# Kernel tuning notes

Hardware: AMD Instinct MI355X
Metric: run time of the kernel (lower is better)

The kernel has to match this reference:

```python
import jax, jax.numpy as jnp
import numpy as np
import math

N_, LQ, C = 8, 300, 256
HEADS, NLVL, NPTS = 8, 4, 8
D_HEAD = C // HEADS
LEVELS = [(128, 128), (64, 64), (32, 32), (16, 16)]
LEN_IN = sum(h * w for h, w in LEVELS)
STARTS = np.cumsum([0] + [h * w for h, w in LEVELS])
MH, MW = 128, 128  # reference mask resolution


def _offset_bias():
    # replicates _reset_parameters grid init for sampling_offsets.bias
    thetas = np.arange(HEADS, dtype=np.float32) * (2.0 * math.pi / HEADS)
    grid = np.stack([np.cos(thetas), np.sin(thetas)], -1)  # (H, 2)
    grid = grid / np.abs(grid).max(-1, keepdims=True)
    grid = np.tile(grid[:, None, None, :], (1, NLVL, NPTS, 1))  # (H, L, P, 2)
    for i in range(NPTS):
        grid[:, :, i, :] *= i + 1
    return jnp.asarray(grid.reshape(-1), dtype=jnp.float32)


def setup_inputs() -> dict:
    key = jax.random.key(0)
    ks = jax.random.split(key, 8)
    query = jax.random.normal(ks[0], (N_, LQ, C), dtype=jnp.float32)
    reference_bboxs = jax.random.normal(ks[1], (N_, LQ, 4), dtype=jnp.float32)
    reference_masks = jax.random.normal(ks[2], (N_, LQ, MH, MW), dtype=jnp.float32)
    input_flatten = jax.random.normal(ks[3], (N_, LEN_IN, C), dtype=jnp.float32)
    input_spatial_shapes = jnp.asarray(LEVELS, dtype=jnp.int64)
    input_level_start_index = jnp.asarray(STARTS[:-1], dtype=jnp.int64)
    input_padding_mask = jnp.zeros((N_, LEN_IN), dtype=bool)
    s = 1.0 / math.sqrt(C)
    W_off = jax.random.normal(ks[4], (C, HEADS * NLVL * NPTS * 2), dtype=jnp.float32) * 0.01
    b_off = _offset_bias()
    W_attn = jax.random.normal(ks[5], (C, HEADS * NLVL * NPTS), dtype=jnp.float32) * 0.01
    b_attn = jnp.zeros((HEADS * NLVL * NPTS,), dtype=jnp.float32)
    W_val = jax.random.normal(ks[6], (C, C), dtype=jnp.float32) * s
    b_val = jnp.zeros((C,), dtype=jnp.float32)
    W_out = jax.random.normal(ks[7], (C, C), dtype=jnp.float32) * s
    b_out = jnp.zeros((C,), dtype=jnp.float32)
    return dict(query=query, reference_bboxs=reference_bboxs, reference_masks=reference_masks,
                mask_threshold=0, input_flatten=input_flatten,
                input_spatial_shapes=input_spatial_shapes,
                input_level_start_index=input_level_start_index,
                input_padding_mask=input_padding_mask,
                W_off=W_off, b_off=b_off, W_attn=W_attn, b_attn=b_attn,
                W_val=W_val, b_val=b_val, W_out=W_out, b_out=b_out)


def get_bounding_boxes(masks):
    # masks: (N, Q, H, W) bool -> normalized (cx, cy, w, h), (N, Q, 4)
    H, W = masks.shape[-2:]
    xs = masks.any(-2)  # (N, Q, W)
    ys = masks.any(-1)  # (N, Q, H)
    xi = jnp.arange(W, dtype=jnp.float32)
    yi = jnp.arange(H, dtype=jnp.float32)
    x_min = jnp.min(jnp.where(xs, xi, float(W)), -1)
    x_max = jnp.max(jnp.where(xs, xi, -1.0), -1)
    y_min = jnp.min(jnp.where(ys, yi, float(H)), -1)
    y_max = jnp.max(jnp.where(ys, yi, -1.0), -1)
    nonempty = xs.any(-1)
    x0, x1 = x_min / W, (x_max + 1.0) / W
    y0, y1 = y_min / H, (y_max + 1.0) / H
    box = jnp.stack([(x0 + x1) * 0.5, (y0 + y1) * 0.5, x1 - x0, y1 - y0], -1)
    return jnp.where(nonempty[..., None], box, 0.0)


def check_points_in_mask(mask, points):
    # mask: (N, Q, H, W) bool; points: (N, Q, P, 2) normalized -> (N, Q, P) float
    N, Q, H, W = mask.shape
    px = jnp.clip((points[..., 0] * W).astype(jnp.int32), 0, W - 1)
    py = jnp.clip((points[..., 1] * H).astype(jnp.int32), 0, H - 1)
    idx = py * W + px  # (N, Q, P)
    flat = mask.reshape(N, Q, H * W)
    return jnp.take_along_axis(flat, idx, axis=2).astype(jnp.float32)


def ms_deform_attn_core(value, sampling_locations, attention_weights):
    # value: (N, Len_in, heads, d); loc: (N, Lq, heads, L, P, 2); w: (N, Lq, heads, L, P)
    N, Lq = sampling_locations.shape[:2]
    out = jnp.zeros((N, Lq, HEADS, D_HEAD), dtype=value.dtype)
    for l, (Hl, Wl) in enumerate(LEVELS):
        v = value[:, STARTS[l]:STARTS[l + 1]].transpose(0, 2, 1, 3)  # (N, heads, Hl*Wl, d)
        loc = sampling_locations[:, :, :, l]  # (N, Lq, heads, P, 2)
        # grid_sample(align_corners=False): pixel = loc*size - 0.5
        px = loc[..., 0] * Wl - 0.5
        py = loc[..., 1] * Hl - 0.5
        x0 = jnp.floor(px); y0 = jnp.floor(py)
        wx1 = px - x0; wy1 = py - y0
        x0i = x0.astype(jnp.int32); y0i = y0.astype(jnp.int32)

        def gather(xi, yi):
            valid = (xi >= 0) & (xi < Wl) & (yi >= 0) & (yi < Hl)
            idx = jnp.clip(yi, 0, Hl - 1) * Wl + jnp.clip(xi, 0, Wl - 1)  # (N, Lq, heads, P)
            idx2 = idx.transpose(0, 2, 1, 3).reshape(N, HEADS, Lq * NPTS)
            g = jnp.take_along_axis(v, idx2[..., None], axis=2)  # (N, heads, Lq*P, d)
            g = g.reshape(N, HEADS, Lq, NPTS, D_HEAD).transpose(0, 2, 1, 3, 4)
            return g * valid[..., None].astype(g.dtype)

        samp = (gather(x0i, y0i) * ((1 - wx1) * (1 - wy1))[..., None]
                + gather(x0i + 1, y0i) * (wx1 * (1 - wy1))[..., None]
                + gather(x0i, y0i + 1) * ((1 - wx1) * wy1)[..., None]
                + gather(x0i + 1, y0i + 1) * (wx1 * wy1)[..., None])
        out = out + jnp.einsum('nqhpd,nqhp->nqhd', samp, attention_weights[:, :, :, l])
    return out.reshape(N, Lq, C)


def reference(query, reference_bboxs, reference_masks, mask_threshold, input_flatten,
              input_spatial_shapes, input_level_start_index, input_padding_mask,
              W_off, b_off, W_attn, b_attn, W_val, b_val, W_out, b_out):
    N, Lq, _ = query.shape
    value = input_flatten @ W_val + b_val
    value = jnp.where(input_padding_mask[..., None], 0.0, value)
    value = value.reshape(N, LEN_IN, HEADS, D_HEAD)
    offsets = (query @ W_off + b_off).reshape(N, Lq, HEADS, NLVL, NPTS, 2)
    attw = (query @ W_attn + b_attn).reshape(N, Lq, HEADS, NLVL, NPTS)
    ref_masks = reference_masks > 0
    box = get_bounding_boxes(ref_masks)  # (N, Lq, 4) normalized cxcywh
    ctr = box[:, :, None, None, None, :2]
    wh = box[:, :, None, None, None, 2:]
    loc = ctr + offsets / NPTS * wh * 0.5  # (N, Lq, heads, L, P, 2)
    pin = check_points_in_mask(ref_masks, loc.reshape(N, Lq, -1, 2))
    attw = attw * pin.reshape(N, Lq, HEADS, NLVL, NPTS)
    attw = jax.nn.softmax(attw.reshape(N, Lq, HEADS, NLVL * NPTS), -1)
    attw = attw.reshape(N, Lq, HEADS, NLVL, NPTS)
    out = ms_deform_attn_core(value, loc, attw)
    return out @ W_out + b_out
```

## Files before the change

kernel.cpp:

```cpp
#include <hip/hip_runtime.h>
#include <math.h>

#define NB    8
#define LQ    300
#define CC    256
#define HEADS 8
#define NLVL  4
#define NPTS  8
#define DH    32
#define LEN_IN 21760
#define NQ    (NB*LQ)
#define MH    128
#define MW    128

typedef __attribute__((ext_vector_type(8))) short bf16x8;
typedef __attribute__((ext_vector_type(8))) unsigned short ushort8;
typedef __attribute__((ext_vector_type(4))) float f32x4;
typedef unsigned short ushort;
typedef unsigned int uint;

#define AS1 __attribute__((address_space(1)))
#define AS3 __attribute__((address_space(3)))

static __device__ __forceinline__ ushort f2bf(float f) {
    uint u = __builtin_bit_cast(uint, f);
    uint r = (u + 0x7fffu + ((u >> 16) & 1u)) >> 16;
    return (ushort)r;
}

__global__ void transpose_cast_w(const float* __restrict__ W, ushort* __restrict__ Bt) {
    int n = blockIdx.x, k = threadIdx.x;
    Bt[n * CC + k] = f2bf(W[(size_t)k * CC + n]);
}

__global__ __launch_bounds__(256) void gemm_mfma_value(
    const float* __restrict__ A, const ushort* __restrict__ Bt,
    const float* __restrict__ bias, float* __restrict__ C, int M)
{
    __shared__ ushort As[128 * 32];
    __shared__ ushort Bs[128 * 32];
    const int tid  = threadIdx.x;
    const int wave = tid >> 6, lane = tid & 63;
    const int bm = blockIdx.x * 128;
    const int bn = blockIdx.y * 128;
    const int wm = (wave >> 1) * 64, wn = (wave & 1) * 64;

    f32x4 acc[4][4] = {};

    const int am = tid >> 1, ak = (tid & 1) * 16;
    const float* aptr = A + (size_t)(bm + am) * CC + ak;
    ushort* as_dst = &As[am * 32 + ak];

    AS3 char* bs_base = (AS3 char*)Bs;

    const int fr = lane & 15, kg = lane >> 4;

    for (int kt = 0; kt < 8; ++kt) {
        const float* ap = aptr + kt * 32;
        float4 f0 = *(const float4*)(ap + 0);
        float4 f1 = *(const float4*)(ap + 4);
        float4 f2 = *(const float4*)(ap + 8);
        float4 f3 = *(const float4*)(ap + 12);
        ushort8 u0, u1;
        u0[0]=f2bf(f0.x); u0[1]=f2bf(f0.y); u0[2]=f2bf(f0.z); u0[3]=f2bf(f0.w);
        u0[4]=f2bf(f1.x); u0[5]=f2bf(f1.y); u0[6]=f2bf(f1.z); u0[7]=f2bf(f1.w);
        u1[0]=f2bf(f2.x); u1[1]=f2bf(f2.y); u1[2]=f2bf(f2.z); u1[3]=f2bf(f2.w);
        u1[4]=f2bf(f3.x); u1[5]=f2bf(f3.y); u1[6]=f2bf(f3.z); u1[7]=f2bf(f3.w);
        *(ushort8*)(as_dst + 0) = u0;
        *(ushort8*)(as_dst + 8) = u1;
        #pragma unroll
        for (int j = 0; j < 2; ++j) {
            int c = wave * 128 + j * 64 + lane;
            const ushort* g = Bt + (size_t)(bn + (c >> 2)) * CC + kt * 32 + (c & 3) * 8;
            __builtin_amdgcn_global_load_lds((const AS1 void*)g,
                                             (AS3 void*)(bs_base + (wave * 128 + j * 64) * 16),
                                             16, 0, 0);
        }
        __syncthreads();
        bf16x8 af[4], bfv[4];
        #pragma unroll
        for (int i = 0; i < 4; ++i)
            af[i] = *(const bf16x8*)&As[(wm + i * 16 + fr) * 32 + kg * 8];
        #pragma unroll
        for (int j = 0; j < 4; ++j)
            bfv[j] = *(const bf16x8*)&Bs[(wn + j * 16 + fr) * 32 + kg * 8];
        #pragma unroll
        for (int i = 0; i < 4; ++i)
            #pragma unroll
            for (int j = 0; j < 4; ++j)
                acc[i][j] = __builtin_amdgcn_mfma_f32_16x16x32_bf16(af[i], bfv[j], acc[i][j], 0, 0, 0);
        __syncthreads();
    }

    const int col0 = lane & 15, rq = (lane >> 4) * 4;
    #pragma unroll
    for (int j = 0; j < 4; ++j) {
        const int col = bn + wn + j * 16 + col0;
        const float bv = bias[col];
        #pragma unroll
        for (int i = 0; i < 4; ++i) {
            const int row = bm + wm + i * 16 + rq;
            #pragma unroll
            for (int r = 0; r < 4; ++r)
                C[(size_t)(row + r) * CC + col] = acc[i][j][r] + bv;
        }
    }
}

#define TM 64
#define TN 64
#define TK 16

__global__ __launch_bounds__(256) void gemm_bias_kernel(
    const float* __restrict__ A, const float* __restrict__ B,
    const float* __restrict__ bias, float* __restrict__ Cmat,
    int M, int N, int K)
{
    __shared__ float As[TK][TM + 4];
    __shared__ float Bs[TK][TN + 4];
    const int tid = threadIdx.x;
    const int bm = blockIdx.x * TM;
    const int bn = blockIdx.y * TN;
    const int tm = (tid >> 4) << 2;
    const int tn = (tid & 15) << 2;
    float acc[4][4] = {};

    for (int k0 = 0; k0 < K; k0 += TK) {
        #pragma unroll
        for (int i = 0; i < 4; ++i) {
            int idx = tid + i * 256;
            int m = idx >> 4;
            int k = idx & 15;
            int gm = bm + m;
            float v = 0.f;
            if (gm < M) v = A[(size_t)gm * K + k0 + k];
            As[k][m] = v;
        }
        #pragma unroll
        for (int i = 0; i < 4; ++i) {
            int idx = tid + i * 256;
            int k = idx >> 6;
            int n = idx & 63;
            int gn = bn + n;
            float v = 0.f;
            if (gn < N) v = B[(size_t)(k0 + k) * N + gn];
            Bs[k][n] = v;
        }
        __syncthreads();
        #pragma unroll
        for (int k = 0; k < TK; ++k) {
            float a[4], b[4];
            #pragma unroll
            for (int i = 0; i < 4; ++i) a[i] = As[k][tm + i];
            #pragma unroll
            for (int j = 0; j < 4; ++j) b[j] = Bs[k][tn + j];
            #pragma unroll
            for (int i = 0; i < 4; ++i)
                #pragma unroll
                for (int j = 0; j < 4; ++j)
                    acc[i][j] = fmaf(a[i], b[j], acc[i][j]);
        }
        __syncthreads();
    }

    #pragma unroll
    for (int i = 0; i < 4; ++i) {
        int m = bm + tm + i;
        if (m >= M) continue;
        #pragma unroll
        for (int j = 0; j < 4; ++j) {
            int n = bn + tn + j;
            if (n < N) Cmat[(size_t)m * N + n] = acc[i][j] + bias[n];
        }
    }
}

__global__ __launch_bounds__(256) void fused_sample_kernel(
    const float* __restrict__ masks,
    const float* __restrict__ value,
    const float* __restrict__ offs,
    const float* __restrict__ attw,
    float* __restrict__ samp)
{
    const int b   = blockIdx.x;
    const int n   = b / LQ;
    const int tid = threadIdx.x;
    const float* mask = masks + (size_t)b * (MH * MW);

    int wmin = MW, wmax = -1, hmin = MH, hmax = -1;
    const float4* m4 = (const float4*)mask;
    for (int i = tid; i < (MH * MW) / 4; i += 256) {
        float4 v = m4[i];
        int base = i << 2;
        int h = base >> 7;
        int w0 = base & 127;
        bool a0 = v.x > 0.f, a1 = v.y > 0.f, a2 = v.z > 0.f, a3 = v.w > 0.f;
        if (a0 | a1 | a2 | a3) { hmin = min(hmin, h); hmax = max(hmax, h); }
        if (a0) { wmin = min(wmin, w0);     wmax = max(wmax, w0);     }
        if (a1) { wmin = min(wmin, w0 + 1); wmax = max(wmax, w0 + 1); }
        if (a2) { wmin = min(wmin, w0 + 2); wmax = max(wmax, w0 + 2); }
        if (a3) { wmin = min(wmin, w0 + 3); wmax = max(wmax, w0 + 3); }
    }
    #pragma unroll
    for (int off = 32; off; off >>= 1) {
        wmin = min(wmin, __shfl_xor(wmin, off));
        wmax = max(wmax, __shfl_xor(wmax, off));
        hmin = min(hmin, __shfl_xor(hmin, off));
        hmax = max(hmax, __shfl_xor(hmax, off));
    }
    __shared__ int s_wmin[4], s_wmax[4], s_hmin[4], s_hmax[4];
    __shared__ float s_box[4];
    const int wave = tid >> 6;
    if ((tid & 63) == 0) {
        s_wmin[wave] = wmin; s_wmax[wave] = wmax;
        s_hmin[wave] = hmin; s_hmax[wave] = hmax;
    }
    __syncthreads();
    if (tid == 0) {
        int a = MW, bx = -1, c = MH, d = -1;
        for (int i = 0; i < 4; ++i) {
            a = min(a, s_wmin[i]); bx = max(bx, s_wmax[i]);
            c = min(c, s_hmin[i]); d = max(d, s_hmax[i]);
        }
        if (bx >= 0) {
            float x0 = a * (1.f / MW), x1 = (bx + 1) * (1.f / MW);
            float y0 = c * (1.f / MH), y1 = (d + 1) * (1.f / MH);
            s_box[0] = (x0 + x1) * 0.5f;
            s_box[1] = (y0 + y1) * 0.5f;
            s_box[2] = x1 - x0;
            s_box[3] = y1 - y0;
        } else {
            s_box[0] = s_box[1] = s_box[2] = s_box[3] = 0.f;
        }
    }
    __syncthreads();
    const float cx = s_box[0], cy = s_box[1], whx = s_box[2], why = s_box[3];

    const float ox = offs[(size_t)b * 512 + tid * 2 + 0];
    const float oy = offs[(size_t)b * 512 + tid * 2 + 1];
    const float lx = cx + ox * (1.f / NPTS) * whx * 0.5f;
    const float ly = cy + oy * (1.f / NPTS) * why * 0.5f;
    int px = (int)(lx * MW); px = min(max(px, 0), MW - 1);
    int py = (int)(ly * MH); py = min(max(py, 0), MH - 1);
    const float pin = (mask[py * MW + px] > 0.f) ? 1.f : 0.f;
    const float logit = attw[(size_t)b * 256 + tid] * pin;
    float mx = logit;
    #pragma unroll
    for (int off = 16; off; off >>= 1) mx = fmaxf(mx, __shfl_xor(mx, off, 32));
    const float e = expf(logit - mx);
    float ssum = e;
    #pragma unroll
    for (int off = 16; off; off >>= 1) ssum += __shfl_xor(ssum, off, 32);
    const float w = e / ssum;

    __shared__ float s_lx[256], s_ly[256], s_w[256];
    s_lx[tid] = lx; s_ly[tid] = ly; s_w[tid] = w;
    __syncthreads();

    const int h = tid >> 5, d = tid & 31;
    const int dims[4]   = {128, 64, 32, 16};
    const int starts[4] = {0, 16384, 20480, 21504};
    const float* vbase = value + (size_t)n * LEN_IN * CC + h * DH + d;
    float acc = 0.f;
    #pragma unroll
    for (int l = 0; l < NLVL; ++l) {
        const int Hl = dims[l], Wl = dims[l], st = starts[l];
        #pragma unroll
        for (int p = 0; p < NPTS; ++p) {
            const int pt = (h * NLVL + l) * NPTS + p;
            const float plx = s_lx[pt], ply = s_ly[pt], pw = s_w[pt];
            const float fx = plx * Wl - 0.5f;
            const float fy = ply * Hl - 0.5f;
            const float x0f = floorf(fx), y0f = floorf(fy);
            const float wx = fx - x0f, wy = fy - y0f;
            const int x0 = (int)x0f, y0 = (int)y0f;
            const int x1 = x0 + 1, y1 = y0 + 1;
            const bool xv0 = (x0 >= 0) && (x0 < Wl);
            const bool xv1 = (x1 >= 0) && (x1 < Wl);
            const bool yv0 = (y0 >= 0) && (y0 < Hl);
            const bool yv1 = (y1 >= 0) && (y1 < Hl);
            float v00 = 0.f, v01 = 0.f, v10 = 0.f, v11 = 0.f;
            if (yv0) {
                const float* row = vbase + (size_t)(st + y0 * Wl) * CC;
                if (xv0) v00 = row[(size_t)x0 * CC];
                if (xv1) v01 = row[(size_t)x1 * CC];
            }
            if (yv1) {
                const float* row = vbase + (size_t)(st + y1 * Wl) * CC;
                if (xv0) v10 = row[(size_t)x0 * CC];
                if (xv1) v11 = row[(size_t)x1 * CC];
            }
            const float bil = v00 * (1.f - wx) * (1.f - wy)
                            + v01 * wx * (1.f - wy)
                            + v10 * (1.f - wx) * wy
                            + v11 * wx * wy;
            acc = fmaf(pw, bil, acc);
        }
    }
    samp[(size_t)b * 256 + tid] = acc;
}

extern "C" void kernel_launch(void* const* d_in, const int* in_sizes, int n_in,
                              void* d_out, int out_size, void* d_ws, size_t ws_size,
                              hipStream_t stream)
{
    const float* query  = (const float*)d_in[0];
    const float* masks  = (const float*)d_in[2];
    const float* flat   = (const float*)d_in[4];
    const float* W_off  = (const float*)d_in[8];
    const float* b_off  = (const float*)d_in[9];
    const float* W_attn = (const float*)d_in[10];
    const float* b_attn = (const float*)d_in[11];
    const float* W_val  = (const float*)d_in[12];
    const float* b_val  = (const float*)d_in[13];
    const float* W_out  = (const float*)d_in[14];
    const float* b_out  = (const float*)d_in[15];
    float* out = (float*)d_out;

    float*  ws    = (float*)d_ws;
    float*  value = ws;
    float*  offs  = value + (size_t)NB * LEN_IN * CC;
    float*  attw  = offs + (size_t)NQ * 512;
    float*  samp  = attw + (size_t)NQ * 256;
    ushort* Bt    = (ushort*)(samp + (size_t)NQ * 256);

    const int Mval = NB * LEN_IN;

    transpose_cast_w<<<CC, CC, 0, stream>>>(W_val, Bt);
    gemm_mfma_value<<<dim3(Mval / 128, CC / 128), 256, 0, stream>>>(
        flat, Bt, b_val, value, Mval);
    gemm_bias_kernel<<<dim3((NQ + TM - 1) / TM, 512 / TN), 256, 0, stream>>>(
        query, W_off, b_off, offs, NQ, 512, CC);
    gemm_bias_kernel<<<dim3((NQ + TM - 1) / TM, CC / TN), 256, 0, stream>>>(
        query, W_attn, b_attn, attw, NQ, CC, CC);
    fused_sample_kernel<<<NQ, 256, 0, stream>>>(masks, value, offs, attw, samp);
    gemm_bias_kernel<<<dim3((NQ + TM - 1) / TM, CC / TN), 256, 0, stream>>>(
        samp, W_out, b_out, out, NQ, CC, CC);
}
```

Measured before the change: 679.7 us.

## Store value projection in bf16 and split bbox from sampling with level-parallel threads

The value GEMM now writes its output as bf16 instead of fp32, which halves the writeback of the large value tensor and the gather traffic in the sampler. The fused kernel is split in two. A bbox kernel fully unrolls the mask scan, and a 512-thread sample kernel splits the four levels across two thread halves and combines them through shared memory. Bilinear loads become branchless, using clamped indices and validity weights. Rounding value to bf16 adds precision error in the sampled output.

```diff
diff --git a/kernel.cpp b/kernel.cpp
--- a/kernel.cpp
+++ b/kernel.cpp
@@ -27,6 +27,9 @@
     uint r = (u + 0x7fffu + ((u >> 16) & 1u)) >> 16;
     return (ushort)r;
 }
+static __device__ __forceinline__ float bf2f(ushort u) {
+    return __builtin_bit_cast(float, ((uint)u) << 16);
+}
 
 __global__ void transpose_cast_w(const float* __restrict__ W, ushort* __restrict__ Bt) {
     int n = blockIdx.x, k = threadIdx.x;
@@ -35,7 +38,7 @@
 
 __global__ __launch_bounds__(256) void gemm_mfma_value(
     const float* __restrict__ A, const ushort* __restrict__ Bt,
-    const float* __restrict__ bias, float* __restrict__ C, int M)
+    const float* __restrict__ bias, ushort* __restrict__ C, int M)
 {
     __shared__ ushort As[128 * 32];
     __shared__ ushort Bs[128 * 32];
@@ -50,9 +53,7 @@
     const int am = tid >> 1, ak = (tid & 1) * 16;
     const float* aptr = A + (size_t)(bm + am) * CC + ak;
     ushort* as_dst = &As[am * 32 + ak];
-
     AS3 char* bs_base = (AS3 char*)Bs;
-
     const int fr = lane & 15, kg = lane >> 4;
 
     for (int kt = 0; kt < 8; ++kt) {
@@ -102,7 +103,7 @@
             const int row = bm + wm + i * 16 + rq;
             #pragma unroll
             for (int r = 0; r < 4; ++r)
-                C[(size_t)(row + r) * CC + col] = acc[i][j][r] + bv;
+                C[(size_t)(row + r) * CC + col] = f2bf(acc[i][j][r] + bv);
         }
     }
 }
@@ -175,21 +176,17 @@
     }
 }
 
-__global__ __launch_bounds__(256) void fused_sample_kernel(
-    const float* __restrict__ masks,
-    const float* __restrict__ value,
-    const float* __restrict__ offs,
-    const float* __restrict__ attw,
-    float* __restrict__ samp)
+__global__ __launch_bounds__(256) void bbox_kernel(
+    const float* __restrict__ masks, float* __restrict__ boxes)
 {
     const int b   = blockIdx.x;
-    const int n   = b / LQ;
     const int tid = threadIdx.x;
-    const float* mask = masks + (size_t)b * (MH * MW);
+    const float4* m4 = (const float4*)(masks + (size_t)b * (MH * MW));
 
     int wmin = MW, wmax = -1, hmin = MH, hmax = -1;
-    const float4* m4 = (const float4*)mask;
-    for (int i = tid; i < (MH * MW) / 4; i += 256) {
+    #pragma unroll
+    for (int it = 0; it < 16; ++it) {
+        int i = tid + it * 256;
         float4 v = m4[i];
         int base = i << 2;
         int h = base >> 7;
@@ -209,7 +206,6 @@
         hmax = max(hmax, __shfl_xor(hmax, off));
     }
     __shared__ int s_wmin[4], s_wmax[4], s_hmin[4], s_hmax[4];
-    __shared__ float s_box[4];
     const int wave = tid >> 6;
     if ((tid & 63) == 0) {
         s_wmin[wave] = wmin; s_wmax[wave] = wmax;
@@ -218,86 +214,113 @@
     __syncthreads();
     if (tid == 0) {
         int a = MW, bx = -1, c = MH, d = -1;
+        #pragma unroll
         for (int i = 0; i < 4; ++i) {
             a = min(a, s_wmin[i]); bx = max(bx, s_wmax[i]);
             c = min(c, s_hmin[i]); d = max(d, s_hmax[i]);
         }
+        float4 box;
         if (bx >= 0) {
             float x0 = a * (1.f / MW), x1 = (bx + 1) * (1.f / MW);
             float y0 = c * (1.f / MH), y1 = (d + 1) * (1.f / MH);
-            s_box[0] = (x0 + x1) * 0.5f;
-            s_box[1] = (y0 + y1) * 0.5f;
-            s_box[2] = x1 - x0;
-            s_box[3] = y1 - y0;
+            box = make_float4((x0 + x1) * 0.5f, (y0 + y1) * 0.5f, x1 - x0, y1 - y0);
         } else {
-            s_box[0] = s_box[1] = s_box[2] = s_box[3] = 0.f;
-        }
+            box = make_float4(0.f, 0.f, 0.f, 0.f);
+        }
+        *(float4*)(boxes + (size_t)b * 4) = box;
+    }
+}
+
+template<int WL>
+static __device__ __forceinline__ float sample_level(
+    const ushort* __restrict__ vbase, int st,
+    const float* __restrict__ s_lx, const float* __restrict__ s_ly,
+    const float* __restrict__ s_w, int ptbase)
+{
+    float acc = 0.f;
+    #pragma unroll
+    for (int p = 0; p < NPTS; ++p) {
+        const int pt = ptbase + p;
+        const float fx = s_lx[pt] * WL - 0.5f;
+        const float fy = s_ly[pt] * WL - 0.5f;
+        const float pw = s_w[pt];
+        const float x0f = floorf(fx), y0f = floorf(fy);
+        const float wx = fx - x0f, wy = fy - y0f;
+        const int x0 = (int)x0f, y0 = (int)y0f;
+        const int x1 = x0 + 1, y1 = y0 + 1;
+        const int x0c = min(max(x0, 0), WL - 1);
+        const int x1c = min(max(x1, 0), WL - 1);
+        const int y0c = min(max(y0, 0), WL - 1);
+        const int y1c = min(max(y1, 0), WL - 1);
+        const float vx0 = (x0 >= 0 && x0 < WL) ? 1.f : 0.f;
+        const float vx1 = (x1 >= 0 && x1 < WL) ? 1.f : 0.f;
+        const float vy0 = (y0 >= 0 && y0 < WL) ? 1.f : 0.f;
+        const float vy1 = (y1 >= 0 && y1 < WL) ? 1.f : 0.f;
+        const ushort* r0 = vbase + (size_t)(st + y0c * WL) * CC;
+        const ushort* r1 = vbase + (size_t)(st + y1c * WL) * CC;
+        const float v00 = bf2f(r0[(size_t)x0c * CC]);
+        const float v01 = bf2f(r0[(size_t)x1c * CC]);
+        const float v10 = bf2f(r1[(size_t)x0c * CC]);
+        const float v11 = bf2f(r1[(size_t)x1c * CC]);
+        const float w00 = vx0 * vy0 * (1.f - wx) * (1.f - wy);
+        const float w01 = vx1 * vy0 * wx * (1.f - wy);
+        const float w10 = vx0 * vy1 * (1.f - wx) * wy;
+        const float w11 = vx1 * vy1 * wx * wy;
+        acc += pw * (w00 * v00 + w01 * v01 + w10 * v10 + w11 * v11);
+    }
+    return acc;
+}
+
+__global__ __launch_bounds__(512) void sample_kernel(
+    const float* __restrict__ masks,
+    const ushort* __restrict__ value,
+    const float* __restrict__ offs,
+    const float* __restrict__ attw,
+    const float* __restrict__ boxes,
+    float* __restrict__ samp)
+{
+    const int b   = blockIdx.x;
+    const int n   = b / LQ;
+    const int tid = threadIdx.x;
+
+    __shared__ float s_lx[256], s_ly[256], s_w[256], s_acc[256];
+
+    if (tid < 256) {
+        const float4 box = *(const float4*)(boxes + (size_t)b * 4);
+        const float ox = offs[(size_t)b * 512 + tid * 2 + 0];
+        const float oy = offs[(size_t)b * 512 + tid * 2 + 1];
+        const float lx = box.x + ox * (1.f / NPTS) * box.z * 0.5f;
+        const float ly = box.y + oy * (1.f / NPTS) * box.w * 0.5f;
+        int px = (int)(lx * MW); px = min(max(px, 0), MW - 1);
+        int py = (int)(ly * MH); py = min(max(py, 0), MH - 1);
+        const float pin = (masks[(size_t)b * (MH * MW) + py * MW + px] > 0.f) ? 1.f : 0.f;
+        const float logit = attw[(size_t)b * 256 + tid] * pin;
+        float mx = logit;
+        #pragma unroll
+        for (int off = 16; off; off >>= 1) mx = fmaxf(mx, __shfl_xor(mx, off, 32));
+        const float e = expf(logit - mx);
+        float ssum = e;
+        #pragma unroll
+        for (int off = 16; off; off >>= 1) ssum += __shfl_xor(ssum, off, 32);
+        s_lx[tid] = lx; s_ly[tid] = ly; s_w[tid] = e / ssum;
     }
     __syncthreads();
-    const float cx = s_box[0], cy = s_box[1], whx = s_box[2], why = s_box[3];
-
-    const float ox = offs[(size_t)b * 512 + tid * 2 + 0];
-    const float oy = offs[(size_t)b * 512 + tid * 2 + 1];
-    const float lx = cx + ox * (1.f / NPTS) * whx * 0.5f;
-    const float ly = cy + oy * (1.f / NPTS) * why * 0.5f;
-    int px = (int)(lx * MW); px = min(max(px, 0), MW - 1);
-    int py = (int)(ly * MH); py = min(max(py, 0), MH - 1);
-    const float pin = (mask[py * MW + px] > 0.f) ? 1.f : 0.f;
-    const float logit = attw[(size_t)b * 256 + tid] * pin;
-    float mx = logit;
-    #pragma unroll
-    for (int off = 16; off; off >>= 1) mx = fmaxf(mx, __shfl_xor(mx, off, 32));
-    const float e = expf(logit - mx);
-    float ssum = e;
-    #pragma unroll
-    for (int off = 16; off; off >>= 1) ssum += __shfl_xor(ssum, off, 32);
-    const float w = e / ssum;
-
-    __shared__ float s_lx[256], s_ly[256], s_w[256];
-    s_lx[tid] = lx; s_ly[tid] = ly; s_w[tid] = w;
+
+    const int half = tid >> 8;
+    const int h = (tid >> 5) & 7, d = tid & 31;
+    const ushort* vbase = value + (size_t)n * LEN_IN * CC + h * DH + d;
+    float acc;
+    if (half == 0) {
+        acc  = sample_level<128>(vbase, 0,     s_lx, s_ly, s_w, (h * NLVL + 0) * NPTS);
+        acc += sample_level< 64>(vbase, 16384, s_lx, s_ly, s_w, (h * NLVL + 1) * NPTS);
+        s_acc[tid] = acc;
+    } else {
+        acc  = sample_level< 32>(vbase, 20480, s_lx, s_ly, s_w, (h * NLVL + 2) * NPTS);
+        acc += sample_level< 16>(vbase, 21504, s_lx, s_ly, s_w, (h * NLVL + 3) * NPTS);
+    }
     __syncthreads();
-
-    const int h = tid >> 5, d = tid & 31;
-    const int dims[4]   = {128, 64, 32, 16};
-    const int starts[4] = {0, 16384, 20480, 21504};
-    const float* vbase = value + (size_t)n * LEN_IN * CC + h * DH + d;
-    float acc = 0.f;
-    #pragma unroll
-    for (int l = 0; l < NLVL; ++l) {
-        const int Hl = dims[l], Wl = dims[l], st = starts[l];
-        #pragma unroll
-        for (int p = 0; p < NPTS; ++p) {
-            const int pt = (h * NLVL + l) * NPTS + p;
-            const float plx = s_lx[pt], ply = s_ly[pt], pw = s_w[pt];
-            const float fx = plx * Wl - 0.5f;
-            const float fy = ply * Hl - 0.5f;
-            const float x0f = floorf(fx), y0f = floorf(fy);
-            const float wx = fx - x0f, wy = fy - y0f;
-            const int x0 = (int)x0f, y0 = (int)y0f;
-            const int x1 = x0 + 1, y1 = y0 + 1;
-            const bool xv0 = (x0 >= 0) && (x0 < Wl);
-            const bool xv1 = (x1 >= 0) && (x1 < Wl);
-            const bool yv0 = (y0 >= 0) && (y0 < Hl);
-            const bool yv1 = (y1 >= 0) && (y1 < Hl);
-            float v00 = 0.f, v01 = 0.f, v10 = 0.f, v11 = 0.f;
-            if (yv0) {
-                const float* row = vbase + (size_t)(st + y0 * Wl) * CC;
-                if (xv0) v00 = row[(size_t)x0 * CC];
-                if (xv1) v01 = row[(size_t)x1 * CC];
-            }
-            if (yv1) {
-                const float* row = vbase + (size_t)(st + y1 * Wl) * CC;
-                if (xv0) v10 = row[(size_t)x0 * CC];
-                if (xv1) v11 = row[(size_t)x1 * CC];
-            }
-            const float bil = v00 * (1.f - wx) * (1.f - wy)
-                            + v01 * wx * (1.f - wy)
-                            + v10 * (1.f - wx) * wy
-                            + v11 * wx * wy;
-            acc = fmaf(pw, bil, acc);
-        }
-    }
-    samp[(size_t)b * 256 + tid] = acc;
+    if (half == 1)
+        samp[(size_t)b * 256 + (tid - 256)] = acc + s_acc[tid - 256];
 }
 
 extern "C" void kernel_launch(void* const* d_in, const int* in_sizes, int n_in,
@@ -317,12 +340,12 @@
     const float* b_out  = (const float*)d_in[15];
     float* out = (float*)d_out;
 
-    float*  ws    = (float*)d_ws;
-    float*  value = ws;
-    float*  offs  = value + (size_t)NB * LEN_IN * CC;
+    float*  offs  = (float*)d_ws;
     float*  attw  = offs + (size_t)NQ * 512;
     float*  samp  = attw + (size_t)NQ * 256;
-    ushort* Bt    = (ushort*)(samp + (size_t)NQ * 256);
+    float*  boxes = samp + (size_t)NQ * 256;
+    ushort* value = (ushort*)(boxes + (size_t)NQ * 4);
+    ushort* Bt    = value + (size_t)NB * LEN_IN * CC;
 
     const int Mval = NB * LEN_IN;
 
@@ -333,7 +356,8 @@
         query, W_off, b_off, offs, NQ, 512, CC);
     gemm_bias_kernel<<<dim3((NQ + TM - 1) / TM, CC / TN), 256, 0, stream>>>(
         query, W_attn, b_attn, attw, NQ, CC, CC);
-    fused_sample_kernel<<<NQ, 256, 0, stream>>>(masks, value, offs, attw, samp);
+    bbox_kernel<<<NQ, 256, 0, stream>>>(masks, boxes);
+    sample_kernel<<<NQ, 512, 0, stream>>>(masks, value, offs, attw, boxes, samp);
     gemm_bias_kernel<<<dim3((NQ + TM - 1) / TM, CC / TN), 256, 0, stream>>>(
         samp, W_out, b_out, out, NQ, CC, CC);
 }
```

New measurement: 580.6 us. -14.6%, faster.
